# Kernel optimization log

Measured on AMD Instinct MI355X. Metric: run time of the kernel, lower is better.

## Reference

```python
import jax, jax.numpy as jnp
import numpy as np

B, D = 4, 4            # batch, days
N = 5000               # node_number
V = 256                # congestion_space_dimension
F = 64                 # in_channels
C = 32                 # out_channels per head
H = 4                  # heads
E = 80000              # edges per graph (before self loops)
NEG_SLOPE = 0.2        # PyG GATConv default negative_slope


def setup_inputs() -> dict:
    key = jax.random.key(0)
    ks = jax.random.split(key, 7)
    x = jax.random.randint(ks[0], (B, D, N), 0, V)
    adjacency = jax.random.randint(ks[1], (2, E), 0, N)
    emb = jax.random.normal(ks[2], (V, F), dtype=jnp.float32)
    W = jax.random.normal(ks[3], (F, H * C), dtype=jnp.float32) * 0.1
    att_src = jax.random.normal(ks[4], (H, C), dtype=jnp.float32) * 0.1
    att_dst = jax.random.normal(ks[5], (H, C), dtype=jnp.float32) * 0.1
    bias = jnp.zeros((H * C,), dtype=jnp.float32)
    return {"x": x, "adjacency": adjacency, "emb": emb, "W": W,
            "att_src": att_src, "att_dst": att_dst, "bias": bias}


def reference(x, adjacency, emb, W, att_src, att_dst, bias):
    G = B * D
    feats = emb[x].reshape(G, N, F)                       # [G,N,F] embedding lookup
    # PyG GATConv adds self loops by default
    loops = jnp.arange(N)
    src = jnp.concatenate([adjacency[0], loops])          # [Et]
    dst = jnp.concatenate([adjacency[1], loops])          # [Et]
    xw = jnp.einsum('gnf,fk->gnk', feats, W).reshape(G, N, H, C)
    a_s = jnp.einsum('gnhc,hc->gnh', xw, att_src)         # [G,N,H]
    a_d = jnp.einsum('gnhc,hc->gnh', xw, att_dst)
    e = jax.nn.leaky_relu(a_s[:, src] + a_d[:, dst], NEG_SLOPE)  # [G,Et,H]
    # per-destination segment softmax (stable)
    seg_max = jax.vmap(lambda v: jax.ops.segment_max(v, dst, num_segments=N))(e)
    alpha = jnp.exp(e - seg_max[:, dst])
    denom = jax.vmap(lambda v: jax.ops.segment_sum(v, dst, num_segments=N))(alpha)
    alpha = alpha / denom[:, dst]                         # [G,Et,H]
    msg = alpha[..., None] * xw[:, src]                   # [G,Et,H,C]
    out = jax.vmap(lambda m: jax.ops.segment_sum(m, dst, num_segments=N))(msg)
    out = out.reshape(G, N, H * C) + bias                 # concat heads + bias
    return out.reshape(B, D, N * H * C)
```

## Files before the change

### kernel.cpp

```cpp
#include <hip/hip_runtime.h>
#include <hip/hip_fp16.h>
#include <math.h>

#define NN 5000
#define GG 16
#define VV 256
#define FF 64
#define HH 4
#define CC 32
#define HC 128
#define EE 80000
#define NEG 0.2f
#define CAP 96

__global__ void k_tables(const float* __restrict__ emb, const float* __restrict__ W,
                         const float* __restrict__ att_src, const float* __restrict__ att_dst,
                         __half* __restrict__ T16, float* __restrict__ as_t,
                         float* __restrict__ ad_t,
                         int* __restrict__ cursor, int* __restrict__ csr) {
  if (blockIdx.x >= VV) {
    int n = (blockIdx.x - VV) * 128 + threadIdx.x;
    if (n < NN) {
      cursor[n] = 1;
      csr[n * CAP] = n;
    }
    return;
  }
  __shared__ float se[FF];
  __shared__ float sT[HC];
  const int v = blockIdx.x;
  const int k = threadIdx.x;
  if (k < FF) se[k] = emb[v * FF + k];
  __syncthreads();
  float acc = 0.f;
#pragma unroll
  for (int f = 0; f < FF; ++f) acc += se[f] * W[f * HC + k];
  T16[v * HC + k] = __float2half(acc);
  sT[k] = acc;
  __syncthreads();
  if (k < 2 * HH) {
    const int h = k >> 1;
    const float* att = (k & 1) ? att_dst : att_src;
    float s = 0.f;
#pragma unroll
    for (int c = 0; c < CC; ++c) s += sT[h * CC + c] * att[h * CC + c];
    if (k & 1) ad_t[v * HH + h] = s;
    else       as_t[v * HH + h] = s;
  }
}

#define NSCAT ((EE + 255) / 256)
__global__ void k_scatter_p(const int* __restrict__ src, const int* __restrict__ dst,
                            int* __restrict__ cursor, int* __restrict__ csr,
                            const float* __restrict__ as_t, const float* __restrict__ ad_t,
                            float* __restrict__ P) {
  if (blockIdx.x < NSCAT) {
    int e = blockIdx.x * 256 + threadIdx.x;
    if (e < EE) {
      int d = dst[e];
      int pos = atomicAdd(&cursor[d], 1);
      if (pos < CAP) csr[d * CAP + pos] = src[e];
    }
    return;
  }
  const int d = blockIdx.x - NSCAT;
  const int v = threadIdx.x;
  const float4 a = ((const float4*)as_t)[v];
  const float4 b = ((const float4*)ad_t)[d];
  float e0 = a.x + b.x; e0 = e0 > 0.f ? e0 : NEG * e0;
  float e1 = a.y + b.y; e1 = e1 > 0.f ? e1 : NEG * e1;
  float e2 = a.z + b.z; e2 = e2 > 0.f ? e2 : NEG * e2;
  float e3 = a.w + b.w; e3 = e3 > 0.f ? e3 : NEG * e3;
  float4 p;
  p.x = __expf(e0); p.y = __expf(e1); p.z = __expf(e2); p.w = __expf(e3);
  ((float4*)P)[d * VV + v] = p;
}

__global__ __launch_bounds__(256)
void k_gat(const int* __restrict__ x, const int* __restrict__ cursor,
           const int* __restrict__ csr, const __half* __restrict__ T16,
           const float* __restrict__ P, const float* __restrict__ bias,
           float* __restrict__ out) {
  const int tid  = threadIdx.x;
  const int wave = tid >> 6;
  const int lane = tid & 63;
  const int t    = blockIdx.x * 4 + wave;
  const int n    = t >> 3;
  const int gp   = t & 7;
  const int g    = gp * 2 + (lane >> 5);
  const int cl   = lane & 31;
  const int c4   = cl * 4;
  const int head = cl >> 3;

  const int base = n * CAP;
  const int deg  = min(cursor[n], CAP);
  const int* __restrict__ xg = x + g * NN;
  const int xd   = xg[n];
  const float* __restrict__ Pg = P + ((size_t)xd << 10) + head;

  float4 acc = make_float4(0.f, 0.f, 0.f, 0.f);
  float dsum = 0.f;

#pragma unroll 2
  for (int j = 0; j < deg; ++j) {
    const int srcn = csr[base + j];
    const int xv   = xg[srcn];
    const float p  = Pg[(size_t)xv << 2];
    union { uint2 u; __half2 h2[2]; } tt;
    tt.u = *(const uint2*)&T16[((size_t)xv << 7) + c4];
    const float2 lo = __half22float2(tt.h2[0]);
    const float2 hi = __half22float2(tt.h2[1]);
    acc.x += p * lo.x; acc.y += p * lo.y;
    acc.z += p * hi.x; acc.w += p * hi.y;
    dsum += p;
  }

  const float r = 1.f / dsum;
  const float4 b4 = ((const float4*)bias)[cl];
  float4 o;
  o.x = acc.x * r + b4.x; o.y = acc.y * r + b4.y;
  o.z = acc.z * r + b4.z; o.w = acc.w * r + b4.w;
  *(float4*)&out[((size_t)(g * NN + n)) * HC + c4] = o;
}

extern "C" void kernel_launch(void* const* d_in, const int* in_sizes, int n_in,
                              void* d_out, int out_size, void* d_ws, size_t ws_size,
                              hipStream_t stream) {
  const int*   x       = (const int*)d_in[0];
  const int*   adj     = (const int*)d_in[1];
  const float* emb     = (const float*)d_in[2];
  const float* W       = (const float*)d_in[3];
  const float* att_src = (const float*)d_in[4];
  const float* att_dst = (const float*)d_in[5];
  const float* bias    = (const float*)d_in[6];
  float*       out     = (float*)d_out;

  const int* adj_src = adj;
  const int* adj_dst = adj + EE;

  char* wp = (char*)d_ws;
  __half* T16 = (__half*)wp; wp += (size_t)VV * HC * 2;
  float* as_t = (float*)wp;  wp += (size_t)VV * HH * 4;
  float* ad_t = (float*)wp;  wp += (size_t)VV * HH * 4;
  int* cursor = (int*)wp;    wp += (size_t)NN * 4;
  int* csr    = (int*)wp;    wp += (size_t)NN * CAP * 4;
  float* P    = (float*)wp;  wp += (size_t)VV * VV * HH * 4;

  const int initblk = (NN + 127) / 128;
  k_tables<<<VV + initblk, 128, 0, stream>>>(emb, W, att_src, att_dst,
                                             T16, as_t, ad_t, cursor, csr);
  k_scatter_p<<<NSCAT + VV, 256, 0, stream>>>(adj_src, adj_dst, cursor, csr,
                                              as_t, ad_t, P);
  k_gat<<<NN * 8 / 4, 256, 0, stream>>>(x, cursor, csr, T16, P, bias, out);
}
```

Baseline: 135.3 us.

## Transpose x to node-major, one block per node, shuffle-broadcast CSR

```diff
diff --git a/kernel.cpp b/kernel.cpp
--- a/kernel.cpp
+++ b/kernel.cpp
@@ -50,10 +50,12 @@
 }
 
 #define NSCAT ((EE + 255) / 256)
+#define NXT   ((GG * NN + 255) / 256)
 __global__ void k_scatter_p(const int* __restrict__ src, const int* __restrict__ dst,
                             int* __restrict__ cursor, int* __restrict__ csr,
                             const float* __restrict__ as_t, const float* __restrict__ ad_t,
-                            float* __restrict__ P) {
+                            float* __restrict__ P,
+                            const int* __restrict__ x, int* __restrict__ xT) {
   if (blockIdx.x < NSCAT) {
     int e = blockIdx.x * 256 + threadIdx.x;
     if (e < EE) {
@@ -63,64 +65,92 @@
     }
     return;
   }
-  const int d = blockIdx.x - NSCAT;
-  const int v = threadIdx.x;
-  const float4 a = ((const float4*)as_t)[v];
-  const float4 b = ((const float4*)ad_t)[d];
-  float e0 = a.x + b.x; e0 = e0 > 0.f ? e0 : NEG * e0;
-  float e1 = a.y + b.y; e1 = e1 > 0.f ? e1 : NEG * e1;
-  float e2 = a.z + b.z; e2 = e2 > 0.f ? e2 : NEG * e2;
-  float e3 = a.w + b.w; e3 = e3 > 0.f ? e3 : NEG * e3;
-  float4 p;
-  p.x = __expf(e0); p.y = __expf(e1); p.z = __expf(e2); p.w = __expf(e3);
-  ((float4*)P)[d * VV + v] = p;
+  if (blockIdx.x < NSCAT + VV) {
+    const int d = blockIdx.x - NSCAT;
+    const int v = threadIdx.x;
+    const float4 a = ((const float4*)as_t)[v];
+    const float4 b = ((const float4*)ad_t)[d];
+    float e0 = a.x + b.x; e0 = e0 > 0.f ? e0 : NEG * e0;
+    float e1 = a.y + b.y; e1 = e1 > 0.f ? e1 : NEG * e1;
+    float e2 = a.z + b.z; e2 = e2 > 0.f ? e2 : NEG * e2;
+    float e3 = a.w + b.w; e3 = e3 > 0.f ? e3 : NEG * e3;
+    float4 p;
+    p.x = __expf(e0); p.y = __expf(e1); p.z = __expf(e2); p.w = __expf(e3);
+    ((float4*)P)[d * VV + v] = p;
+    return;
+  }
+  const int i = (blockIdx.x - NSCAT - VV) * 256 + threadIdx.x;
+  if (i < GG * NN) {
+    const int n = i >> 4, g = i & 15;
+    xT[i] = x[g * NN + n];
+  }
 }
 
 __global__ __launch_bounds__(256)
-void k_gat(const int* __restrict__ x, const int* __restrict__ cursor,
+void k_gat(const int* __restrict__ xT, const int* __restrict__ cursor,
            const int* __restrict__ csr, const __half* __restrict__ T16,
            const float* __restrict__ P, const float* __restrict__ bias,
            float* __restrict__ out) {
   const int tid  = threadIdx.x;
-  const int wave = tid >> 6;
+  const int n    = blockIdx.x;
+  const int g    = tid >> 4;
+  const int sl   = tid & 15;
+  const int head = sl >> 2;
   const int lane = tid & 63;
-  const int t    = blockIdx.x * 4 + wave;
-  const int n    = t >> 3;
-  const int gp   = t & 7;
-  const int g    = gp * 2 + (lane >> 5);
-  const int cl   = lane & 31;
-  const int c4   = cl * 4;
-  const int head = cl >> 3;
 
   const int base = n * CAP;
   const int deg  = min(cursor[n], CAP);
-  const int* __restrict__ xg = x + g * NN;
-  const int xd   = xg[n];
+  const int xd   = xT[n * 16 + g];
   const float* __restrict__ Pg = P + ((size_t)xd << 10) + head;
 
-  float4 acc = make_float4(0.f, 0.f, 0.f, 0.f);
+  const int my_csr = csr[base + lane];
+
+  float4 a_lo = make_float4(0.f, 0.f, 0.f, 0.f);
+  float4 a_hi = make_float4(0.f, 0.f, 0.f, 0.f);
   float dsum = 0.f;
 
+  const int d0 = min(deg, 64);
 #pragma unroll 2
-  for (int j = 0; j < deg; ++j) {
+  for (int j = 0; j < d0; ++j) {
+    const int srcn = __shfl(my_csr, j);
+    const int xv   = xT[(srcn << 4) + g];
+    const float p  = Pg[xv << 2];
+    union { uint4 u; __half2 h2[4]; } tt;
+    tt.u = *(const uint4*)&T16[((size_t)xv << 7) + sl * 8];
+    const float2 f0 = __half22float2(tt.h2[0]);
+    const float2 f1 = __half22float2(tt.h2[1]);
+    const float2 f2 = __half22float2(tt.h2[2]);
+    const float2 f3 = __half22float2(tt.h2[3]);
+    a_lo.x += p * f0.x; a_lo.y += p * f0.y; a_lo.z += p * f1.x; a_lo.w += p * f1.y;
+    a_hi.x += p * f2.x; a_hi.y += p * f2.y; a_hi.z += p * f3.x; a_hi.w += p * f3.y;
+    dsum += p;
+  }
+  for (int j = 64; j < deg; ++j) {
     const int srcn = csr[base + j];
-    const int xv   = xg[srcn];
-    const float p  = Pg[(size_t)xv << 2];
-    union { uint2 u; __half2 h2[2]; } tt;
-    tt.u = *(const uint2*)&T16[((size_t)xv << 7) + c4];
-    const float2 lo = __half22float2(tt.h2[0]);
-    const float2 hi = __half22float2(tt.h2[1]);
-    acc.x += p * lo.x; acc.y += p * lo.y;
-    acc.z += p * hi.x; acc.w += p * hi.y;
+    const int xv   = xT[(srcn << 4) + g];
+    const float p  = Pg[xv << 2];
+    union { uint4 u; __half2 h2[4]; } tt;
+    tt.u = *(const uint4*)&T16[((size_t)xv << 7) + sl * 8];
+    const float2 f0 = __half22float2(tt.h2[0]);
+    const float2 f1 = __half22float2(tt.h2[1]);
+    const float2 f2 = __half22float2(tt.h2[2]);
+    const float2 f3 = __half22float2(tt.h2[3]);
+    a_lo.x += p * f0.x; a_lo.y += p * f0.y; a_lo.z += p * f1.x; a_lo.w += p * f1.y;
+    a_hi.x += p * f2.x; a_hi.y += p * f2.y; a_hi.z += p * f3.x; a_hi.w += p * f3.y;
     dsum += p;
   }
 
   const float r = 1.f / dsum;
-  const float4 b4 = ((const float4*)bias)[cl];
-  float4 o;
-  o.x = acc.x * r + b4.x; o.y = acc.y * r + b4.y;
-  o.z = acc.z * r + b4.z; o.w = acc.w * r + b4.w;
-  *(float4*)&out[((size_t)(g * NN + n)) * HC + c4] = o;
+  const float4 b_lo = ((const float4*)bias)[sl * 2];
+  const float4 b_hi = ((const float4*)bias)[sl * 2 + 1];
+  float4 o0, o1;
+  o0.x = a_lo.x * r + b_lo.x; o0.y = a_lo.y * r + b_lo.y;
+  o0.z = a_lo.z * r + b_lo.z; o0.w = a_lo.w * r + b_lo.w;
+  o1.x = a_hi.x * r + b_hi.x; o1.y = a_hi.y * r + b_hi.y;
+  o1.z = a_hi.z * r + b_hi.z; o1.w = a_hi.w * r + b_hi.w;
+  float* op = out + ((size_t)(g * NN + n)) * HC + sl * 8;
+  *(float4*)op = o0;
+  *(float4*)(op + 4) = o1;
 }
 
 extern "C" void kernel_launch(void* const* d_in, const int* in_sizes, int n_in,
@@ -145,11 +175,12 @@
   int* cursor = (int*)wp;    wp += (size_t)NN * 4;
   int* csr    = (int*)wp;    wp += (size_t)NN * CAP * 4;
   float* P    = (float*)wp;  wp += (size_t)VV * VV * HH * 4;
+  int* xT     = (int*)wp;    wp += (size_t)GG * NN * 4;
 
   const int initblk = (NN + 127) / 128;
   k_tables<<<VV + initblk, 128, 0, stream>>>(emb, W, att_src, att_dst,
                                              T16, as_t, ad_t, cursor, csr);
-  k_scatter_p<<<NSCAT + VV, 256, 0, stream>>>(adj_src, adj_dst, cursor, csr,
-                                              as_t, ad_t, P);
-  k_gat<<<NN * 8 / 4, 256, 0, stream>>>(x, cursor, csr, T16, P, bias, out);
+  k_scatter_p<<<NSCAT + VV + NXT, 256, 0, stream>>>(adj_src, adj_dst, cursor, csr,
+                                                    as_t, ad_t, P, x, xT);
+  k_gat<<<NN, 256, 0, stream>>>(xT, cursor, csr, T16, P, bias, out);
 }
```

Result: faster. 117.1 us (-13.5%).
